# Kernel tuning notes

Measured on AMD Instinct MI355X. Metric: run time of the kernel, lower is better.

The kernel has to match this reference:

```python
import jax, jax.numpy as jnp
import numpy as np

GROUP = 128

def _dequant(q, s, z):
    # q: [O, K] int4 values in [0,16); s,z: [O, K//GROUP]
    O, K = q.shape
    qg = q.reshape(O, K // GROUP, GROUP)
    w = (qg - z[:, :, None]).astype(s.dtype) * s[:, :, None]
    return w.reshape(O, K)

def setup_inputs() -> dict:
    key = jax.random.key(0)
    ks = jax.random.split(key, 7)
    H, I = 4096, 14336
    x = jax.random.normal(ks[0], (2, 2048, H), jnp.float32)
    q_up = jax.random.randint(ks[1], (I, H), 0, 16, jnp.int32)
    s_up = (jax.random.uniform(ks[2], (I, H // GROUP), jnp.float32) * 0.02 + 1e-3)
    z_up = jax.random.randint(ks[3], (I, H // GROUP), 0, 16, jnp.int32)
    q_down = jax.random.randint(ks[4], (H, I), 0, 16, jnp.int32)
    s_down = (jax.random.uniform(ks[5], (H, I // GROUP), jnp.float32) * 0.02 + 1e-3)
    z_down = jax.random.randint(ks[6], (H, I // GROUP), 0, 16, jnp.int32)
    return {"x": x, "q_up": q_up, "s_up": s_up, "z_up": z_up,
            "q_down": q_down, "s_down": s_down, "z_down": z_down}

def reference(x, q_up, s_up, z_up, q_down, s_down, z_down):
    # up_proj: W4A16 dequant + GEMM, weight layout [out, in] like nn.Linear
    w_up = _dequant(q_up, s_up, z_up)        # [I, H]
    h = jnp.einsum('bsh,ih->bsi', x, w_up)   # [B, S, I]
    # NemotronH 'relu2' activation: relu(h)^2
    a = jnp.square(jax.nn.relu(h))
    w_down = _dequant(q_down, s_down, z_down)  # [H, I]
    y = jnp.einsum('bsi,hi->bsh', a, w_down)   # [B, S, H]
    return y
```

## Files before the change

kernel.cpp:

```cpp
#include <hip/hip_runtime.h>
#include <stdint.h>

typedef unsigned short u16;
typedef __attribute__((ext_vector_type(4))) float f32x4;
typedef __attribute__((ext_vector_type(8))) __bf16 bf16x8;
typedef __attribute__((ext_vector_type(8))) unsigned short u16x8;

__device__ __forceinline__ u16 f2bf(float f) {
  unsigned u = __builtin_bit_cast(unsigned, f);
  u = (u + 0x7fffu + ((u >> 16) & 1u)) >> 16;
  return (u16)u;
}

typedef __attribute__((address_space(1))) const void gvoid_t;
typedef __attribute__((address_space(3))) void lvoid_t;

__device__ __forceinline__ void gload_lds16(const void* g, void* l) {
  __builtin_amdgcn_global_load_lds((gvoid_t*)g, (lvoid_t*)l, 16, 0, 0);
}

__global__ __launch_bounds__(256)
void dequant_kernel(const int* __restrict__ q, const float* __restrict__ s,
                    const int* __restrict__ z, u16* __restrict__ w, int K) {
  const int row = blockIdx.y;
  const int k = (blockIdx.x * 256 + threadIdx.x) << 3;
  const int ng = K >> 7;
  const int g = k >> 7;
  const float sv = s[(size_t)row * ng + g];
  const float zv = (float)z[(size_t)row * ng + g];
  const int4* qp = (const int4*)(q + (size_t)row * K + k);
  const int4 a = qp[0], b = qp[1];
  u16x8 o;
  o[0] = f2bf(((float)a.x - zv) * sv);
  o[1] = f2bf(((float)a.y - zv) * sv);
  o[2] = f2bf(((float)a.z - zv) * sv);
  o[3] = f2bf(((float)a.w - zv) * sv);
  o[4] = f2bf(((float)b.x - zv) * sv);
  o[5] = f2bf(((float)b.y - zv) * sv);
  o[6] = f2bf(((float)b.z - zv) * sv);
  o[7] = f2bf(((float)b.w - zv) * sv);
  *reinterpret_cast<u16x8*>(w + (size_t)row * K + k) = o;
}

__global__ __launch_bounds__(256)
void cvt_kernel(const float* __restrict__ in, u16* __restrict__ out) {
  const size_t i = ((size_t)blockIdx.x * 256 + threadIdx.x) << 3;
  const float4* p = (const float4*)(in + i);
  const float4 a = p[0], b = p[1];
  u16x8 o;
  o[0] = f2bf(a.x); o[1] = f2bf(a.y); o[2] = f2bf(a.z); o[3] = f2bf(a.w);
  o[4] = f2bf(b.x); o[5] = f2bf(b.y); o[6] = f2bf(b.z); o[7] = f2bf(b.w);
  *reinterpret_cast<u16x8*>(out + i) = o;
}

template<bool RELU2>
__global__ __launch_bounds__(512, 2)
void gemm256(const u16* __restrict__ Ap, const u16* __restrict__ Bp,
             void* __restrict__ Cptr, int M, int N, int K) {
  __shared__ __align__(16) u16 As[2][256][64];
  __shared__ __align__(16) u16 Bs[2][256][64];
  const int tid = threadIdx.x;
  const int lane = tid & 63;
  const int wid = tid >> 6;
  const int wr = wid >> 2, wc = wid & 3;

  const int nbx = N >> 8;
  const int nwg = gridDim.x;
  int bid = blockIdx.x;
  bid = (bid & 7) * (nwg >> 3) + (bid >> 3);
  const int m0 = (bid / nbx) << 8;
  const int n0 = (bid % nbx) << 8;

  const int srow = tid >> 3;
  const int scol = tid & 7;
  const int lr = lane & 15;
  const int lk = (lane >> 4) << 3;
  const int xorc = (lr & 7) << 3;

  f32x4 acc[8][4] = {};
  bf16x8 a1[4], a2[4], a3[4], a4[4], b1[4], b2[4];

  const int nk = K >> 6;

#define STG_A(bufi, h, kt) do { _Pragma("unroll") \
  for (int l_ = 0; l_ < 2; ++l_) { \
    const int r_ = (h) * 128 + l_ * 64 + srow; \
    gload_lds16(Ap + (size_t)(m0 + r_) * K + (size_t)((kt) << 6) + ((scol ^ (srow & 7)) << 3), \
                &As[bufi][r_][scol << 3]); } } while (0)
#define STG_B(bufi, h, kt) do { _Pragma("unroll") \
  for (int l_ = 0; l_ < 2; ++l_) { \
    const int r_ = (h) * 128 + l_ * 64 + srow; \
    gload_lds16(Bp + (size_t)(n0 + r_) * K + (size_t)((kt) << 6) + ((scol ^ (srow & 7)) << 3), \
                &Bs[bufi][r_][scol << 3]); } } while (0)
#define RD_A(bufi, ks, half, dst) do { _Pragma("unroll") \
  for (int i_ = 0; i_ < 4; ++i_) { \
    const int row_ = wr * 128 + ((half) * 4 + i_) * 16 + lr; \
    dst[i_] = *reinterpret_cast<const bf16x8*>(&As[bufi][row_][((ks) * 32 + lk) ^ xorc]); } } while (0)
#define RD_B(bufi, ks, dst) do { _Pragma("unroll") \
  for (int j_ = 0; j_ < 4; ++j_) { \
    const int row_ = wc * 64 + j_ * 16 + lr; \
    dst[j_] = *reinterpret_cast<const bf16x8*>(&Bs[bufi][row_][((ks) * 32 + lk) ^ xorc]); } } while (0)
#define MFMA16(ASET, BSET, I0) do { _Pragma("unroll") \
  for (int i_ = 0; i_ < 4; ++i_) { _Pragma("unroll") \
    for (int j_ = 0; j_ < 4; ++j_) \
      acc[(I0) + i_][j_] = __builtin_amdgcn_mfma_f32_16x16x32_bf16( \
        ASET[i_], BSET[j_], acc[(I0) + i_][j_], 0, 0, 0); } } while (0)
#define BARO() do { asm volatile("" ::: "memory"); __builtin_amdgcn_s_barrier(); \
  asm volatile("" ::: "memory"); } while (0)
#define PH(GATEOP, Q) do { \
  BARO(); \
  asm volatile("s_waitcnt lgkmcnt(0)" ::: "memory"); \
  __builtin_amdgcn_sched_barrier(0); \
  __builtin_amdgcn_s_setprio(1); Q; __builtin_amdgcn_s_setprio(0); \
  GATEOP; \
  BARO(); \
} while (0)
#define NOGATE do {} while (0)
#define GATE4 asm volatile("s_waitcnt vmcnt(4)" ::: "memory")
#define TILE4(p, S1, S2, S3, S4) do { \
  RD_A(p, 0, 0, a1); RD_B(p, 0, b1); S1; PH(NOGATE, MFMA16(a1, b1, 0)); \
  RD_A(p, 0, 1, a2); RD_A(p, 1, 1, a4); RD_A(p, 1, 0, a3); S2; PH(NOGATE, MFMA16(a2, b1, 4)); \
  RD_B(p, 1, b2); S3; PH(NOGATE, MFMA16(a4, b2, 4)); \
  S4; PH(GATE4, MFMA16(a3, b2, 0)); } while (0)

  STG_A(0, 0, 0); STG_A(0, 1, 0);
  STG_B(0, 0, 0); STG_B(0, 1, 0);
  STG_A(1, 0, 1); STG_A(1, 1, 1);
  asm volatile("s_waitcnt vmcnt(4)" ::: "memory");
  BARO();

  const int nit = nk >> 1;
  for (int it = 0; it < nit; ++it) {
    const int t1 = 2 * it + 1;
    int t2 = 2 * it + 2; if (t2 >= nk) t2 -= nk;
    int t3 = 2 * it + 3; if (t3 >= nk) t3 -= nk;
    TILE4(0, STG_B(1, 0, t1), STG_B(1, 1, t1), STG_A(0, 0, t2), STG_A(0, 1, t2));
    TILE4(1, STG_B(0, 0, t2), STG_B(0, 1, t2), STG_A(1, 0, t3), STG_A(1, 1, t3));
  }
  asm volatile("s_waitcnt vmcnt(0)" ::: "memory");

  const int crow = (lane >> 4) << 2;
  const int ccol = lane & 15;
#pragma unroll
  for (int i = 0; i < 8; ++i) {
#pragma unroll
    for (int j = 0; j < 4; ++j) {
#pragma unroll
      for (int q = 0; q < 4; ++q) {
        const int m = m0 + wr * 128 + i * 16 + crow + q;
        const int n = n0 + wc * 64 + j * 16 + ccol;
        const float v = acc[i][j][q];
        if constexpr (RELU2) {
          const float r = fmaxf(v, 0.f);
          ((u16*)Cptr)[(size_t)m * N + n] = f2bf(r * r);
        } else {
          ((float*)Cptr)[(size_t)m * N + n] = v;
        }
      }
    }
  }
#undef STG_A
#undef STG_B
#undef RD_A
#undef RD_B
#undef MFMA16
#undef BARO
#undef PH
#undef NOGATE
#undef GATE4
#undef TILE4
}

extern "C" void kernel_launch(void* const* d_in, const int* in_sizes, int n_in,
                              void* d_out, int out_size, void* d_ws, size_t ws_size,
                              hipStream_t stream) {
  const float* x    = (const float*)d_in[0];
  const int*   q_up = (const int*)d_in[1];
  const float* s_up = (const float*)d_in[2];
  const int*   z_up = (const int*)d_in[3];
  const int*   q_dn = (const int*)d_in[4];
  const float* s_dn = (const float*)d_in[5];
  const int*   z_dn = (const int*)d_in[6];
  float* y = (float*)d_out;

  const int H = 4096, I = 14336;
  const int M = in_sizes[0] / H;

  const size_t wbytes = (size_t)I * H * 2;
  const size_t abytes = (size_t)M * I * 2;
  const size_t xbytes = (size_t)M * H * 2;
  u16* wbuf = (u16*)d_ws;
  u16* abuf = (u16*)((char*)d_ws + wbytes);
  u16* xbf  = (u16*)((char*)d_ws + wbytes + abytes);
  if (ws_size < wbytes + abytes + xbytes) return;

  dequant_kernel<<<dim3(H / 8 / 256, I), 256, 0, stream>>>(q_up, s_up, z_up, wbuf, H);
  cvt_kernel<<<dim3((int)(((size_t)M * H) >> 11)), 256, 0, stream>>>(x, xbf);
  gemm256<true><<<dim3((M / 256) * (I / 256)), 512, 0, stream>>>(xbf, wbuf, abuf, M, I, H);
  dequant_kernel<<<dim3(I / 8 / 256, H), 256, 0, stream>>>(q_dn, s_dn, z_dn, wbuf, I);
  gemm256<false><<<dim3((M / 256) * (H / 256)), 512, 0, stream>>>(abuf, wbuf, y, M, H, I);
}
```

Before: 1.086 ms.

## Restructure GEMM main loop to overlap LDS reads with MFMA using partial lgkmcnt waits

Rewrites the per-tile schedule of the bf16 GEMM. LDS fragment reads for later phases are now issued before earlier MFMA groups, with staged lgkmcnt(8/4/0) waits, instead of a full wait inside each phase. The number of barriers per tile drops from eight to four. LDS addresses use precomputed byte base pointers and an XOR offset, and A/B prefetch staging is swapped. The aim is to hide LDS latency behind matrix math and cut synchronization cost, at the risk of buffer-reuse races and higher register pressure.

Measured after the change: 952.3 us. 1.14x faster.

```diff
diff --git a/kernel.cpp b/kernel.cpp
--- a/kernel.cpp
+++ b/kernel.cpp
@@ -77,6 +77,12 @@
   const int lk = (lane >> 4) << 3;
   const int xorc = (lr & 7) << 3;
 
+  const char* baA0 = (const char*)&As[0][0][0] + (wr * 128 + lr) * 128;
+  const char* baA1 = baA0 + 32768;
+  const char* baB0 = (const char*)&Bs[0][0][0] + (wc * 64 + lr) * 128;
+  const char* baB1 = baB0 + 32768;
+  const int koff0 = (lk ^ xorc) * 2;
+
   f32x4 acc[8][4] = {};
   bf16x8 a1[4], a2[4], a3[4], a4[4], b1[4], b2[4];
 
@@ -92,14 +98,14 @@
     const int r_ = (h) * 128 + l_ * 64 + srow; \
     gload_lds16(Bp + (size_t)(n0 + r_) * K + (size_t)((kt) << 6) + ((scol ^ (srow & 7)) << 3), \
                 &Bs[bufi][r_][scol << 3]); } } while (0)
-#define RD_A(bufi, ks, half, dst) do { _Pragma("unroll") \
-  for (int i_ = 0; i_ < 4; ++i_) { \
-    const int row_ = wr * 128 + ((half) * 4 + i_) * 16 + lr; \
-    dst[i_] = *reinterpret_cast<const bf16x8*>(&As[bufi][row_][((ks) * 32 + lk) ^ xorc]); } } while (0)
-#define RD_B(bufi, ks, dst) do { _Pragma("unroll") \
-  for (int j_ = 0; j_ < 4; ++j_) { \
-    const int row_ = wc * 64 + j_ * 16 + lr; \
-    dst[j_] = *reinterpret_cast<const bf16x8*>(&Bs[bufi][row_][((ks) * 32 + lk) ^ xorc]); } } while (0)
+#define RD_A(base, ks, half, dst) do { _Pragma("unroll") \
+  for (int i_ = 0; i_ < 4; ++i_) \
+    dst[i_] = *reinterpret_cast<const bf16x8*>( \
+      (base) + ((half) * 4 + i_) * 2048 + (koff0 ^ ((ks) * 64))); } while (0)
+#define RD_B(base, ks, dst) do { _Pragma("unroll") \
+  for (int j_ = 0; j_ < 4; ++j_) \
+    dst[j_] = *reinterpret_cast<const bf16x8*>( \
+      (base) + j_ * 2048 + (koff0 ^ ((ks) * 64))); } while (0)
 #define MFMA16(ASET, BSET, I0) do { _Pragma("unroll") \
   for (int i_ = 0; i_ < 4; ++i_) { _Pragma("unroll") \
     for (int j_ = 0; j_ < 4; ++j_) \
@@ -107,35 +113,45 @@
         ASET[i_], BSET[j_], acc[(I0) + i_][j_], 0, 0, 0); } } while (0)
 #define BARO() do { asm volatile("" ::: "memory"); __builtin_amdgcn_s_barrier(); \
   asm volatile("" ::: "memory"); } while (0)
-#define PH(GATEOP, Q) do { \
-  BARO(); \
-  asm volatile("s_waitcnt lgkmcnt(0)" ::: "memory"); \
-  __builtin_amdgcn_sched_barrier(0); \
-  __builtin_amdgcn_s_setprio(1); Q; __builtin_amdgcn_s_setprio(0); \
-  GATEOP; \
-  BARO(); \
+#define LGKM(n) do { asm volatile("s_waitcnt lgkmcnt(" #n ")" ::: "memory"); \
+  __builtin_amdgcn_sched_barrier(0); } while (0)
+#define SB0 __builtin_amdgcn_sched_barrier(0)
+#define GATE4 asm volatile("s_waitcnt vmcnt(4)" ::: "memory")
+#define PRIO(Q) do { __builtin_amdgcn_s_setprio(1); Q; __builtin_amdgcn_s_setprio(0); } while (0)
+#define TILE4(bA, bB, SA1, SA2, SB3, SB4) do { \
+  BARO(); \
+  RD_B(bB, 0, b1); RD_A(bA, 0, 0, a1); \
+  LGKM(0); \
+  SA1; \
+  PRIO(MFMA16(a1, b1, 0)); \
+  SB0; RD_B(bB, 1, b2); SB0; RD_A(bA, 0, 1, a2); SB0; RD_A(bA, 1, 1, a4); SB0; RD_A(bA, 1, 0, a3); \
+  BARO(); \
+  LGKM(8); \
+  SA2; \
+  PRIO(MFMA16(a2, b1, 4)); \
+  BARO(); \
+  LGKM(4); \
+  SB3; \
+  PRIO(MFMA16(a4, b2, 4)); \
+  BARO(); \
+  LGKM(0); \
+  SB4; \
+  PRIO(MFMA16(a3, b2, 0)); \
+  GATE4; \
 } while (0)
-#define NOGATE do {} while (0)
-#define GATE4 asm volatile("s_waitcnt vmcnt(4)" ::: "memory")
-#define TILE4(p, S1, S2, S3, S4) do { \
-  RD_A(p, 0, 0, a1); RD_B(p, 0, b1); S1; PH(NOGATE, MFMA16(a1, b1, 0)); \
-  RD_A(p, 0, 1, a2); RD_A(p, 1, 1, a4); RD_A(p, 1, 0, a3); S2; PH(NOGATE, MFMA16(a2, b1, 4)); \
-  RD_B(p, 1, b2); S3; PH(NOGATE, MFMA16(a4, b2, 4)); \
-  S4; PH(GATE4, MFMA16(a3, b2, 0)); } while (0)
 
   STG_A(0, 0, 0); STG_A(0, 1, 0);
   STG_B(0, 0, 0); STG_B(0, 1, 0);
-  STG_A(1, 0, 1); STG_A(1, 1, 1);
+  STG_B(1, 0, 1); STG_B(1, 1, 1);
   asm volatile("s_waitcnt vmcnt(4)" ::: "memory");
-  BARO();
 
   const int nit = nk >> 1;
   for (int it = 0; it < nit; ++it) {
     const int t1 = 2 * it + 1;
     int t2 = 2 * it + 2; if (t2 >= nk) t2 -= nk;
     int t3 = 2 * it + 3; if (t3 >= nk) t3 -= nk;
-    TILE4(0, STG_B(1, 0, t1), STG_B(1, 1, t1), STG_A(0, 0, t2), STG_A(0, 1, t2));
-    TILE4(1, STG_B(0, 0, t2), STG_B(0, 1, t2), STG_A(1, 0, t3), STG_A(1, 1, t3));
+    TILE4(baA0, baB0, STG_A(1, 0, t1), STG_A(1, 1, t1), STG_B(0, 0, t2), STG_B(0, 1, t2));
+    TILE4(baA1, baB1, STG_A(0, 0, t2), STG_A(0, 1, t2), STG_B(1, 0, t3), STG_B(1, 1, t3));
   }
   asm volatile("s_waitcnt vmcnt(0)" ::: "memory");
 
@@ -165,9 +181,10 @@
 #undef RD_B
 #undef MFMA16
 #undef BARO
-#undef PH
-#undef NOGATE
+#undef LGKM
+#undef SB0
 #undef GATE4
+#undef PRIO
 #undef TILE4
 }
 
```
